# Kernel tuning notes

Hardware: AMD Instinct MI355X
Metric: run time of the kernel (lower is better)

## Reference

```python
import jax, jax.numpy as jnp
import numpy as np

N_EXPERTS = 8
D_IN = 1024
D_OUT = 1024
BATCH = 4096


def setup_inputs() -> dict:
    key = jax.random.key(0)
    k_x, k_w, k_b, k_a = jax.random.split(key, 4)
    xs = jax.random.normal(k_x, (BATCH, D_IN), dtype=jnp.float32)
    mxs = jnp.arange(BATCH, dtype=jnp.int32)  # opaque per-sample metadata, passed through
    actions = jax.random.randint(k_a, (BATCH,), 0, N_EXPERTS, dtype=jnp.int64)
    # Expert parameters: each submodule is Linear(D_IN -> D_OUT)
    W = jax.random.normal(k_w, (N_EXPERTS, D_OUT, D_IN), dtype=jnp.float32) / np.sqrt(D_IN)
    b = jax.random.normal(k_b, (N_EXPERTS, D_OUT), dtype=jnp.float32) * 0.01
    return {"xs": xs, "mxs": mxs, "actions": actions, "W": W, "b": b}


def reference(xs, mxs, actions, W, b):
    # Original: per-sample python loop y_i = submodule[actions[i]](x_i); cat along batch.
    # Vectorized: compute all experts densely (E small), then select per-sample row.
    y_all = jnp.einsum("bj,eij->bei", xs, W) + b[None, :, :]  # [B, E, D_OUT]
    ys = jnp.take_along_axis(y_all, actions[:, None, None].astype(jnp.int32), axis=1)
    ys = jnp.squeeze(ys, axis=1)  # [B, D_OUT]
    return (ys, mxs, actions)
```

## Files before the change

kernel.cpp:

```cpp
#include <hip/hip_runtime.h>

#define BATCH 4096
#define D_IN 1024
#define D_OUT 1024
#define N_EXPERTS 8

#define TM 64
#define TN 128
#define TK 32
#define MAX_TILES 71

#define WS_PERM    0
#define WS_STARTS  4096
#define WS_TILE_E  4112
#define WS_TILE_M  4200
#define WS_NTILES  4288

#define WS_XHI_OFF   32768
#define WS_XLO_OFF   (32768 + 8388608)
#define WS_WHI_OFF   (32768 + 2*8388608)
#define WS_WLO_OFF   (32768 + 2*8388608 + 16777216)
#define WS_NEEDED    (32768 + 2*8388608 + 2*16777216)

typedef __attribute__((ext_vector_type(8))) short short8;
typedef __attribute__((ext_vector_type(4))) float f32x4;

__device__ __forceinline__ void cvt8(const float4 a, const float4 b,
                                     short8& h, short8& l) {
    float f[8] = {a.x, a.y, a.z, a.w, b.x, b.y, b.z, b.w};
#pragma unroll
    for (int i = 0; i < 8; ++i) {
        const unsigned u = __float_as_uint(f[i]);
        h[i] = (short)(u >> 16);
        const float r = f[i] - __uint_as_float(u & 0xffff0000u);
        l[i] = (short)(__float_as_uint(r) >> 16);
    }
}

__global__ __launch_bounds__(256) void prep_kernel(
    const int* __restrict__ actions, const int* __restrict__ mxs,
    const float* __restrict__ xs, const float* __restrict__ W,
    int* __restrict__ ws,
    short* __restrict__ XhiP, short* __restrict__ XloP,
    short* __restrict__ WhiP, short* __restrict__ WloP,
    float* __restrict__ out, int meta_mode)
{
    const int bid = blockIdx.x;
    const int t = threadIdx.x;

    if (bid == 0) {
        __shared__ int chunkoff[64][N_EXPERTS];
        const int lane = t & 63;
        const int wave = t >> 6;

        for (int it = 0; it < 16; ++it) {
            const int c = wave * 16 + it;
            const int a = actions[c * 64 + lane];
            int myc = 0;
#pragma unroll
            for (int e = 0; e < N_EXPERTS; ++e) {
                const unsigned long long me = __ballot(a == e);
                if (lane == e) myc = (int)__popcll(me);
            }
            if (lane < N_EXPERTS) chunkoff[c][lane] = myc;
        }
        __syncthreads();

        if (wave == 0) {
            int cc0 = chunkoff[lane][0], cc1 = chunkoff[lane][1];
            int cc2 = chunkoff[lane][2], cc3 = chunkoff[lane][3];
            int cc4 = chunkoff[lane][4], cc5 = chunkoff[lane][5];
            int cc6 = chunkoff[lane][6], cc7 = chunkoff[lane][7];
            int tot0, tot1, tot2, tot3, tot4, tot5, tot6, tot7;
            int ex0, ex1, ex2, ex3, ex4, ex5, ex6, ex7;
#define SCAN1(CC, TOT, EX) do {                                   \
            int v = CC;                                           \
            _Pragma("unroll")                                     \
            for (int d = 1; d < 64; d <<= 1) {                    \
                const int u = __shfl_up(v, d, 64);                \
                if (lane >= d) v += u;                            \
            }                                                     \
            TOT = __shfl(v, 63, 64);                              \
            EX = v - CC;                                          \
        } while (0)
            SCAN1(cc0, tot0, ex0); SCAN1(cc1, tot1, ex1);
            SCAN1(cc2, tot2, ex2); SCAN1(cc3, tot3, ex3);
            SCAN1(cc4, tot4, ex4); SCAN1(cc5, tot5, ex5);
            SCAN1(cc6, tot6, ex6); SCAN1(cc7, tot7, ex7);
#undef SCAN1
            const int b0 = 0;
            const int b1 = b0 + tot0, b2 = b1 + tot1, b3 = b2 + tot2;
            const int b4 = b3 + tot3, b5 = b4 + tot4, b6 = b5 + tot5;
            const int b7 = b6 + tot6;
            chunkoff[lane][0] = b0 + ex0; chunkoff[lane][1] = b1 + ex1;
            chunkoff[lane][2] = b2 + ex2; chunkoff[lane][3] = b3 + ex3;
            chunkoff[lane][4] = b4 + ex4; chunkoff[lane][5] = b5 + ex5;
            chunkoff[lane][6] = b6 + ex6; chunkoff[lane][7] = b7 + ex7;
            if (lane == 0) {
                ws[WS_STARTS + 0] = b0; ws[WS_STARTS + 1] = b1;
                ws[WS_STARTS + 2] = b2; ws[WS_STARTS + 3] = b3;
                ws[WS_STARTS + 4] = b4; ws[WS_STARTS + 5] = b5;
                ws[WS_STARTS + 6] = b6; ws[WS_STARTS + 7] = b7;
                ws[WS_STARTS + 8] = BATCH;
                int nt = 0;
                int tots[8] = {tot0, tot1, tot2, tot3, tot4, tot5, tot6, tot7};
#pragma unroll
                for (int e = 0; e < N_EXPERTS; ++e)
                    for (int m0 = 0; m0 < tots[e]; m0 += TM) {
                        ws[WS_TILE_E + nt] = e;
                        ws[WS_TILE_M + nt] = m0;
                        ++nt;
                    }
                ws[WS_NTILES] = nt;
            }
        }
        __syncthreads();

        for (int it = 0; it < 16; ++it) {
            const int c = wave * 16 + it;
            const int i = c * 64 + lane;
            const int a = actions[i];
            unsigned long long msel = 0;
#pragma unroll
            for (int e = 0; e < N_EXPERTS; ++e) {
                const unsigned long long me = __ballot(a == e);
                if (a == e) msel = me;
            }
            const int rank = (int)__popcll(msel & ((1ull << lane) - 1ull));
            const int pos = chunkoff[c][a] + rank;
            ws[WS_PERM + pos] = i;
        }
        return;
    }

    if (bid <= 16) {
        const int i = (bid - 1) * 256 + t;
        if (meta_mode == 2) {
            out[BATCH * D_OUT + i] = (float)mxs[i];
            long long* a64 = (long long*)(out + BATCH * D_OUT + BATCH);
            a64[i] = (long long)actions[i];
        } else if (meta_mode == 1) {
            out[BATCH * D_OUT + i] = (float)mxs[i];
            out[BATCH * D_OUT + BATCH + i] = (float)actions[i];
        }
        return;
    }

    const int g = (bid - 17) * 256 + t;
    if (g < 1048576) {
        const int slot = g & 63;
        const int i2   = (g >> 6) & 7;
        const int blk  = g >> 9;
        const int nt   = blk & 7;
        const int kt   = (blk >> 3) & 31;
        const int e    = blk >> 8;
        const int c    = slot & 15;
        const int j    = slot >> 4;
        const int n    = nt * 128 + i2 * 16 + c;
        const float* p = W + ((size_t)(e << 10) + n) * D_IN + kt * 32 + j * 8;
        const float4 f0 = *(const float4*)p;
        const float4 f1 = *(const float4*)(p + 4);
        short8 h, l;
        cvt8(f0, f1, h, l);
        *(short8*)(WhiP + (size_t)g * 8) = h;
        *(short8*)(WloP + (size_t)g * 8) = l;
    } else {
        const int g2 = g - 1048576;
        const float* p = xs + (size_t)g2 * 8;
        const float4 f0 = *(const float4*)p;
        const float4 f1 = *(const float4*)(p + 4);
        short8 h, l;
        cvt8(f0, f1, h, l);
        *(short8*)(XhiP + (size_t)g2 * 8) = h;
        *(short8*)(XloP + (size_t)g2 * 8) = l;
    }
}

__global__ __launch_bounds__(256) void moe_gemm_pc(
    const short* __restrict__ Xhi, const short* __restrict__ Xlo,
    const short* __restrict__ Whi, const short* __restrict__ Wlo,
    const float* __restrict__ bias, const int* __restrict__ ws,
    float* __restrict__ out)
{
    const int tix = blockIdx.y;
    if (tix >= ws[WS_NTILES]) return;
    const int e   = ws[WS_TILE_E + tix];
    const int m0  = ws[WS_TILE_M + tix];
    const int s0  = ws[WS_STARTS + e];
    const int cnt = ws[WS_STARTS + e + 1] - s0;
    const int n0  = blockIdx.x * TN;

    __shared__ short Ahi[2][4 * 512];
    __shared__ short Alo[2][4 * 512];
    __shared__ short Bhi[2][8 * 512];
    __shared__ short Blo[2][8 * 512];
    __shared__ int   rows_s[TM];

    const int t = threadIdx.x;
    if (t < TM) {
        const int r = m0 + t;
        rows_s[t] = (r < cnt) ? ws[WS_PERM + s0 + r] : -1;
    }
    {
        const short8 z = {0, 0, 0, 0, 0, 0, 0, 0};
        ((short8*)&Ahi[0][0])[t] = z;
        ((short8*)&Ahi[1][0])[t] = z;
        ((short8*)&Alo[0][0])[t] = z;
        ((short8*)&Alo[1][0])[t] = z;
    }
    __syncthreads();

    const int lane = t & 63;
    const int wave = t >> 6;
    const int wm = (wave & 1) * 32;
    const int wn = (wave >> 1) * 64;

    const float zf = 0.f;
    f32x4 acc[2][4];
#pragma unroll
    for (int mi = 0; mi < 2; ++mi)
#pragma unroll
        for (int nj = 0; nj < 4; ++nj)
            acc[mi][nj] = (f32x4){zf, zf, zf, zf};

    const int arow = rows_s[wave * 16 + (lane & 15)];
    const bool avalid = arow >= 0;
    const short* aSrcHi = Xhi + (size_t)(avalid ? arow : 0) * D_IN + (lane >> 4) * 8;
    const short* aSrcLo = Xlo + (size_t)(avalid ? arow : 0) * D_IN + (lane >> 4) * 8;

    const size_t wBase = ((size_t)e * 256 + (size_t)blockIdx.x) * 4096;
    const size_t bo0 = (size_t)wave * 512 + lane * 8;
    const size_t bo1 = (size_t)(wave + 4) * 512 + lane * 8;

#define STAGE(KT, BUF) do {                                                    \
        const int _kt = (KT);                                                  \
        if (avalid) {                                                          \
            __builtin_amdgcn_global_load_lds(                                  \
                (const __attribute__((address_space(1))) void*)(aSrcHi + _kt * 32), \
                (__attribute__((address_space(3))) void*)&Ahi[BUF][wave * 512],\
                16, 0, 0);                                                     \
            __builtin_amdgcn_global_load_lds(                                  \
                (const __attribute__((address_space(1))) void*)(aSrcLo + _kt * 32), \
                (__attribute__((address_space(3))) void*)&Alo[BUF][wave * 512],\
                16, 0, 0);                                                     \
        }                                                                      \
        {                                                                      \
            const size_t _wo = wBase + (size_t)_kt * 32768;                    \
            __builtin_amdgcn_global_load_lds(                                  \
                (const __attribute__((address_space(1))) void*)(Whi + _wo + bo0), \
                (__attribute__((address_space(3))) void*)&Bhi[BUF][wave * 512],\
                16, 0, 0);                                                     \
            __builtin_amdgcn_global_load_lds(                                  \
                (const __attribute__((address_space(1))) void*)(Wlo + _wo + bo0), \
                (__attribute__((address_space(3))) void*)&Blo[BUF][wave * 512],\
                16, 0, 0);                                                     \
            __builtin_amdgcn_global_load_lds(                                  \
                (const __attribute__((address_space(1))) void*)(Whi + _wo + bo1), \
                (__attribute__((address_space(3))) void*)&Bhi[BUF][(wave + 4) * 512], \
                16, 0, 0);                                                     \
            __builtin_amdgcn_global_load_lds(                                  \
                (const __attribute__((address_space(1))) void*)(Wlo + _wo + bo1), \
                (__attribute__((address_space(3))) void*)&Blo[BUF][(wave + 4) * 512], \
                16, 0, 0);                                                     \
        }                                                                      \
    } while (0)

    const int rds = lane * 8;

#define FRAG_MFMA(BUF) do {                                                  \
        short8 ah[2], al[2], bh[4], bl[4];                                   \
        _Pragma("unroll")                                                    \
        for (int i2 = 0; i2 < 2; ++i2) {                                     \
            const int aoff = ((wm >> 4) + i2) * 512 + rds;                   \
            ah[i2] = *(const short8*)&Ahi[BUF][aoff];                        \
            al[i2] = *(const short8*)&Alo[BUF][aoff];                        \
        }                                                                    \
        _Pragma("unroll")                                                    \
        for (int i2 = 0; i2 < 4; ++i2) {                                     \
            const int boff = ((wn >> 4) + i2) * 512 + rds;                   \
            bh[i2] = *(const short8*)&Bhi[BUF][boff];                        \
            bl[i2] = *(const short8*)&Blo[BUF][boff];                        \
        }                                                                    \
        _Pragma("unroll")                                                    \
        for (int mi = 0; mi < 2; ++mi)                                       \
            _Pragma("unroll")                                                \
            for (int nj = 0; nj < 4; ++nj) {                                 \
                acc[mi][nj] = __builtin_amdgcn_mfma_f32_16x16x32_bf16(ah[mi], bh[nj], acc[mi][nj], 0, 0, 0); \
                acc[mi][nj] = __builtin_amdgcn_mfma_f32_16x16x32_bf16(ah[mi], bl[nj], acc[mi][nj], 0, 0, 0); \
                acc[mi][nj] = __builtin_amdgcn_mfma_f32_16x16x32_bf16(al[mi], bh[nj], acc[mi][nj], 0, 0, 0); \
            }                                                                \
    } while (0)

#define VBAR() asm volatile("s_waitcnt vmcnt(0) lgkmcnt(0)\n\ts_barrier" ::: "memory")

    STAGE(0, 0);
    VBAR();

    int kt = 1;
#pragma unroll 1
    for (int i = 0; i < 15; ++i) {
        STAGE(kt, 1);
        FRAG_MFMA(0);
        VBAR();
        STAGE(kt + 1, 0);
        FRAG_MFMA(1);
        VBAR();
        kt += 2;
    }
    STAGE(31, 1);
    FRAG_MFMA(0);
    VBAR();
    FRAG_MFMA(1);

#undef STAGE
#undef FRAG_MFMA
#undef VBAR

    const int cl = lane & 15;
    const int qd = lane >> 4;
    float bv[4];
#pragma unroll
    for (int nj = 0; nj < 4; ++nj)
        bv[nj] = bias[e * D_OUT + n0 + wn + nj * 16 + cl];
#pragma unroll
    for (int mi = 0; mi < 2; ++mi) {
#pragma unroll
        for (int reg = 0; reg < 4; ++reg) {
            const int mloc = wm + mi * 16 + qd * 4 + reg;
            const int r = rows_s[mloc];
            if (r >= 0) {
                float* orow = out + (size_t)r * D_OUT + n0 + wn + cl;
#pragma unroll
                for (int nj = 0; nj < 4; ++nj)
                    orow[nj * 16] = acc[mi][nj][reg] + bv[nj];
            }
        }
    }
}

__global__ __launch_bounds__(256) void moe_gemm_fb(
    const float* __restrict__ xs, const float* __restrict__ W,
    const float* __restrict__ bias, const int* __restrict__ ws,
    float* __restrict__ out)
{
    const int tix = blockIdx.y;
    if (tix >= ws[WS_NTILES]) return;
    const int e   = ws[WS_TILE_E + tix];
    const int m0  = ws[WS_TILE_M + tix];
    const int s0  = ws[WS_STARTS + e];
    const int cnt = ws[WS_STARTS + e + 1] - s0;
    const int n0  = blockIdx.x * TN;

    __shared__ short Ahi[2][TM * TK];
    __shared__ short Alo[2][TM * TK];
    __shared__ short Bhi[2][TN * TK];
    __shared__ short Blo[2][TN * TK];
    __shared__ int   rows_s[TM];

    const int t = threadIdx.x;
    if (t < TM) {
        const int r = m0 + t;
        rows_s[t] = (r < cnt) ? ws[WS_PERM + s0 + r] : -1;
    }
    __syncthreads();

    const int lane = t & 63;
    const int wave = t >> 6;
    const int wm = (wave & 1) * 32;
    const int wn = (wave >> 1) * 64;

    const float zf = 0.f;
    f32x4 acc[2][4];
#pragma unroll
    for (int mi = 0; mi < 2; ++mi)
#pragma unroll
        for (int nj = 0; nj < 4; ++nj)
            acc[mi][nj] = (f32x4){zf, zf, zf, zf};

    const float* Wb = W + (size_t)e * (D_OUT * (size_t)D_IN) + (size_t)n0 * D_IN;

    const int j  = t & 3;
    const int rr = t >> 2;

    const int arow = rows_s[rr];
    const float* aptr = (arow >= 0) ? (xs + (size_t)arow * D_IN + j * 8) : nullptr;

    const int slotA   = (j * 16 + (rr & 15)) ^ (j << 1);
    const int aoff_st = (rr >> 4) * 512 + slotA * 8;
    const int boff0   = aoff_st;
    const int boff1   = aoff_st + 4 * 512;

    const float* qb0 = Wb + (size_t)rr * D_IN + j * 8;
    const float* qb1 = Wb + (size_t)(64 + rr) * D_IN + j * 8;

    const int rds = (lane ^ ((lane >> 4) << 1)) * 8;

#define LOAD_SET(A0, A1, B0, B1, B2, B3, KOFF) do {                          \
        const int _k = (KOFF);                                               \
        if (aptr) {                                                          \
            A0 = *(const float4*)(aptr + _k);                                \
            A1 = *(const float4*)(aptr + _k + 4);                            \
        }                                                                    \
        B0 = *(const float4*)(qb0 + _k); B1 = *(const float4*)(qb0 + _k + 4);\
        B2 = *(const float4*)(qb1 + _k); B3 = *(const float4*)(qb1 + _k + 4);\
    } while (0)

#define CVT_STORE_SET(A0, A1, B0, B1, B2, B3, BUF) do {                      \
        short8 _h, _l;                                                       \
        cvt8(A0, A1, _h, _l);                                                \
        *(short8*)&Ahi[BUF][aoff_st] = _h; *(short8*)&Alo[BUF][aoff_st] = _l;\
        cvt8(B0, B1, _h, _l);                                                \
        *(short8*)&Bhi[BUF][boff0] = _h;   *(short8*)&Blo[BUF][boff0] = _l;  \
        cvt8(B2, B3, _h, _l);                                                \
        *(short8*)&Bhi[BUF][boff1] = _h;   *(short8*)&Blo[BUF][boff1] = _l;  \
    } while (0)

#define FRAG_MFMA(BUF) do {                                                  \
        short8 ah[2], al[2], bh[4], bl[4];                                   \
        _Pragma("unroll")                                                    \
        for (int i2 = 0; i2 < 2; ++i2) {                                     \
            const int aoff = ((wm >> 4) + i2) * 512 + rds;                   \
            ah[i2] = *(const short8*)&Ahi[BUF][aoff];                        \
            al[i2] = *(const short8*)&Alo[BUF][aoff];                        \
        }                                                                    \
        _Pragma("unroll")                                                    \
        for (int i2 = 0; i2 < 4; ++i2) {                                     \
            const int boff = ((wn >> 4) + i2) * 512 + rds;                   \
            bh[i2] = *(const short8*)&Bhi[BUF][boff];                        \
            bl[i2] = *(const short8*)&Blo[BUF][boff];                        \
        }                                                                    \
        _Pragma("unroll")                                                    \
        for (int mi = 0; mi < 2; ++mi)                                       \
            _Pragma("unroll")                                                \
            for (int nj = 0; nj < 4; ++nj) {                                 \
                acc[mi][nj] = __builtin_amdgcn_mfma_f32_16x16x32_bf16(ah[mi], bh[nj], acc[mi][nj], 0, 0, 0); \
                acc[mi][nj] = __builtin_amdgcn_mfma_f32_16x16x32_bf16(ah[mi], bl[nj], acc[mi][nj], 0, 0, 0); \
                acc[mi][nj] = __builtin_amdgcn_mfma_f32_16x16x32_bf16(al[mi], bh[nj], acc[mi][nj], 0, 0, 0); \
            }                                                                \
    } while (0)

#define PIPE_BARRIER() asm volatile("s_waitcnt lgkmcnt(0)\n\ts_barrier" ::: "memory")

    float4 ax0 = make_float4(0.f, 0.f, 0.f, 0.f), ax1 = ax0;
    float4 bx0, bx1, bx2, bx3;
    float4 ay0 = make_float4(0.f, 0.f, 0.f, 0.f), ay1 = ay0;
    float4 by0, by1, by2, by3;

    LOAD_SET(ax0, ax1, bx0, bx1, bx2, bx3, 0);
    CVT_STORE_SET(ax0, ax1, bx0, bx1, bx2, bx3, 0);
    LOAD_SET(ax0, ax1, bx0, bx1, bx2, bx3, TK);
    PIPE_BARRIER();

    int ke = 2 * TK;
#pragma unroll 1
    for (int i = 0; i < 15; ++i) {
        {
            LOAD_SET(ay0, ay1, by0, by1, by2, by3, ke);
            FRAG_MFMA(0);
            CVT_STORE_SET(ax0, ax1, bx0, bx1, bx2, bx3, 1);
            PIPE_BARRIER();
        }
        {
            LOAD_SET(ax0, ax1, bx0, bx1, bx2, bx3, ke + TK);
            FRAG_MFMA(1);
            CVT_STORE_SET(ay0, ay1, by0, by1, by2, by3, 0);
            PIPE_BARRIER();
        }
        ke += 2 * TK;
    }
    {
        FRAG_MFMA(0);
        CVT_STORE_SET(ax0, ax1, bx0, bx1, bx2, bx3, 1);
        PIPE_BARRIER();
    }
    {
        FRAG_MFMA(1);
    }

#undef LOAD_SET
#undef CVT_STORE_SET
#undef FRAG_MFMA
#undef PIPE_BARRIER

    const int cl = lane & 15;
    const int qd = lane >> 4;
    float bv[4];
#pragma unroll
    for (int nj = 0; nj < 4; ++nj)
        bv[nj] = bias[e * D_OUT + n0 + wn + nj * 16 + cl];
#pragma unroll
    for (int mi = 0; mi < 2; ++mi) {
#pragma unroll
        for (int reg = 0; reg < 4; ++reg) {
            const int mloc = wm + mi * 16 + qd * 4 + reg;
            const int r = rows_s[mloc];
            if (r >= 0) {
                float* orow = out + (size_t)r * D_OUT + n0 + wn + cl;
#pragma unroll
                for (int nj = 0; nj < 4; ++nj)
                    orow[nj * 16] = acc[mi][nj][reg] + bv[nj];
            }
        }
    }
}

extern "C" void kernel_launch(void* const* d_in, const int* in_sizes, int n_in,
                              void* d_out, int out_size, void* d_ws, size_t ws_size,
                              hipStream_t stream) {
    const float* xs      = (const float*)d_in[0];
    const int*   mxs     = (const int*)d_in[1];
    const int*   actions = (const int*)d_in[2];
    const float* W       = (const float*)d_in[3];
    const float* bias    = (const float*)d_in[4];
    float* out = (float*)d_out;
    int*   ws  = (int*)d_ws;
    char*  wsb = (char*)d_ws;

    short* XhiP = (short*)(wsb + WS_XHI_OFF);
    short* XloP = (short*)(wsb + WS_XLO_OFF);
    short* WhiP = (short*)(wsb + WS_WHI_OFF);
    short* WloP = (short*)(wsb + WS_WLO_OFF);

    const int metaOff = BATCH * D_OUT;
    const int meta_mode = (out_size >= metaOff + 3 * BATCH) ? 2
                        : (out_size >= metaOff + 2 * BATCH) ? 1 : 0;

    const bool big = ws_size >= (size_t)WS_NEEDED;
    const int prep_blocks = big ? (17 + 6144) : 17;

    prep_kernel<<<prep_blocks, 256, 0, stream>>>(
        actions, mxs, xs, W, ws, XhiP, XloP, WhiP, WloP, out, meta_mode);

    dim3 grid(D_OUT / TN, MAX_TILES, 1);
    if (big) {
        moe_gemm_pc<<<grid, 256, 0, stream>>>(XhiP, XloP, WhiP, WloP, bias, ws, out);
    } else {
        moe_gemm_fb<<<grid, 256, 0, stream>>>(xs, W, bias, ws, out);
    }
}
```

Baseline: 153.7 us.

## Deepen GEMM prefetch with partial vmcnt waits and linearize block grid

The main loop now issues loads two k-steps ahead and waits with vmcnt(6) so that one stage's global-to-LDS loads stay in flight while the other buffer is consumed, using a separate LDS read fence before overwriting a buffer. Invalid A rows now load row 0 unconditionally instead of being predicated off, which removes the LDS zero-initialisation and the branch. The grid becomes 1D with the 8 N-slices of a tile adjacent, so blocks sharing the same X rows run close together for better cache reuse. Garbage rows are still masked at store time, but the extra barriers and the reliance on the vmcnt count add some ordering risk.

```diff
diff --git a/kernel.cpp b/kernel.cpp
--- a/kernel.cpp
+++ b/kernel.cpp
@@ -182,13 +182,15 @@
     const float* __restrict__ bias, const int* __restrict__ ws,
     float* __restrict__ out)
 {
-    const int tix = blockIdx.y;
+    const int wid = blockIdx.x;
+    const int nsl = wid & 7;
+    const int tix = wid >> 3;
     if (tix >= ws[WS_NTILES]) return;
     const int e   = ws[WS_TILE_E + tix];
     const int m0  = ws[WS_TILE_M + tix];
     const int s0  = ws[WS_STARTS + e];
     const int cnt = ws[WS_STARTS + e + 1] - s0;
-    const int n0  = blockIdx.x * TN;
+    const int n0  = nsl * TN;
 
     __shared__ short Ahi[2][4 * 512];
     __shared__ short Alo[2][4 * 512];
@@ -201,13 +203,6 @@
         const int r = m0 + t;
         rows_s[t] = (r < cnt) ? ws[WS_PERM + s0 + r] : -1;
     }
-    {
-        const short8 z = {0, 0, 0, 0, 0, 0, 0, 0};
-        ((short8*)&Ahi[0][0])[t] = z;
-        ((short8*)&Ahi[1][0])[t] = z;
-        ((short8*)&Alo[0][0])[t] = z;
-        ((short8*)&Alo[1][0])[t] = z;
-    }
     __syncthreads();
 
     const int lane = t & 63;
@@ -223,27 +218,25 @@
         for (int nj = 0; nj < 4; ++nj)
             acc[mi][nj] = (f32x4){zf, zf, zf, zf};
 
-    const int arow = rows_s[wave * 16 + (lane & 15)];
-    const bool avalid = arow >= 0;
-    const short* aSrcHi = Xhi + (size_t)(avalid ? arow : 0) * D_IN + (lane >> 4) * 8;
-    const short* aSrcLo = Xlo + (size_t)(avalid ? arow : 0) * D_IN + (lane >> 4) * 8;
-
-    const size_t wBase = ((size_t)e * 256 + (size_t)blockIdx.x) * 4096;
+    const int arow0 = rows_s[wave * 16 + (lane & 15)];
+    const int arow  = arow0 < 0 ? 0 : arow0;
+    const short* aSrcHi = Xhi + (size_t)arow * D_IN + (lane >> 4) * 8;
+    const short* aSrcLo = Xlo + (size_t)arow * D_IN + (lane >> 4) * 8;
+
+    const size_t wBase = ((size_t)e * 256 + (size_t)nsl) * 4096;
     const size_t bo0 = (size_t)wave * 512 + lane * 8;
     const size_t bo1 = (size_t)(wave + 4) * 512 + lane * 8;
 
 #define STAGE(KT, BUF) do {                                                    \
         const int _kt = (KT);                                                  \
-        if (avalid) {                                                          \
-            __builtin_amdgcn_global_load_lds(                                  \
-                (const __attribute__((address_space(1))) void*)(aSrcHi + _kt * 32), \
-                (__attribute__((address_space(3))) void*)&Ahi[BUF][wave * 512],\
-                16, 0, 0);                                                     \
-            __builtin_amdgcn_global_load_lds(                                  \
-                (const __attribute__((address_space(1))) void*)(aSrcLo + _kt * 32), \
-                (__attribute__((address_space(3))) void*)&Alo[BUF][wave * 512],\
-                16, 0, 0);                                                     \
-        }                                                                      \
+        __builtin_amdgcn_global_load_lds(                                      \
+            (const __attribute__((address_space(1))) void*)(aSrcHi + _kt * 32),\
+            (__attribute__((address_space(3))) void*)&Ahi[BUF][wave * 512],    \
+            16, 0, 0);                                                         \
+        __builtin_amdgcn_global_load_lds(                                      \
+            (const __attribute__((address_space(1))) void*)(aSrcLo + _kt * 32),\
+            (__attribute__((address_space(3))) void*)&Alo[BUF][wave * 512],    \
+            16, 0, 0);                                                         \
         {                                                                      \
             const size_t _wo = wBase + (size_t)_kt * 32768;                    \
             __builtin_amdgcn_global_load_lds(                                  \
@@ -291,30 +284,36 @@
             }                                                                \
     } while (0)
 
-#define VBAR() asm volatile("s_waitcnt vmcnt(0) lgkmcnt(0)\n\ts_barrier" ::: "memory")
+#define WAIT6_BAR() asm volatile("s_waitcnt vmcnt(6)\n\ts_barrier" ::: "memory")
+#define WAIT0_BAR() asm volatile("s_waitcnt vmcnt(0)\n\ts_barrier" ::: "memory")
+#define READ_FENCE() asm volatile("s_waitcnt lgkmcnt(0)\n\ts_barrier" ::: "memory")
 
     STAGE(0, 0);
-    VBAR();
-
-    int kt = 1;
+    STAGE(1, 1);
+
+    int kt = 2;
 #pragma unroll 1
     for (int i = 0; i < 15; ++i) {
-        STAGE(kt, 1);
+        WAIT6_BAR();
         FRAG_MFMA(0);
-        VBAR();
-        STAGE(kt + 1, 0);
+        READ_FENCE();
+        STAGE(kt, 0);
+        WAIT6_BAR();
         FRAG_MFMA(1);
-        VBAR();
+        READ_FENCE();
+        STAGE(kt + 1, 1);
         kt += 2;
     }
-    STAGE(31, 1);
+    WAIT6_BAR();
     FRAG_MFMA(0);
-    VBAR();
+    WAIT0_BAR();
     FRAG_MFMA(1);
 
 #undef STAGE
 #undef FRAG_MFMA
-#undef VBAR
+#undef WAIT6_BAR
+#undef WAIT0_BAR
+#undef READ_FENCE
 
     const int cl = lane & 15;
     const int qd = lane >> 4;
@@ -531,10 +530,10 @@
     prep_kernel<<<prep_blocks, 256, 0, stream>>>(
         actions, mxs, xs, W, ws, XhiP, XloP, WhiP, WloP, out, meta_mode);
 
-    dim3 grid(D_OUT / TN, MAX_TILES, 1);
     if (big) {
-        moe_gemm_pc<<<grid, 256, 0, stream>>>(XhiP, XloP, WhiP, WloP, bias, ws, out);
+        moe_gemm_pc<<<8 * MAX_TILES, 256, 0, stream>>>(XhiP, XloP, WhiP, WloP, bias, ws, out);
     } else {
+        dim3 grid(D_OUT / TN, MAX_TILES, 1);
         moe_gemm_fb<<<grid, 256, 0, stream>>>(xs, W, bias, ws, out);
     }
 }
```

New measurement: 152.7 us. No clear change (-0.6%).
